# Optimization experiments

Hardware: AMD Instinct MI355X
Metric: run time of the kernel (lower is better)

The kernel has to match this reference:

```python
import jax, jax.numpy as jnp
import numpy as np

N, D, E = 16384, 1024, 8

def setup_inputs() -> dict:
    key = jax.random.key(0)
    ks = jax.random.split(key, 5)
    s = 1.0 / np.sqrt(D)
    return {
        "x": jax.random.normal(ks[0], (N, D), dtype=jnp.float32),
        "router_w": jax.random.uniform(ks[1], (E, D), jnp.float32, -s, s),   # torch Linear weight [out,in]
        "router_b": jax.random.uniform(ks[2], (E,), jnp.float32, -s, s),
        "expert_w": jax.random.uniform(ks[3], (E, D, D), jnp.float32, -s, s),  # [E, out, in]
        "expert_b": jax.random.uniform(ks[4], (E, D), jnp.float32, -s, s),
    }

def reference(x, router_w, router_b, expert_w, expert_b):
    # Router: logits -> softmax -> argmax (argmax of softmax == argmax of logits)
    logits = x @ router_w.T + router_b            # [N, E]
    top = jnp.argmax(logits, axis=-1)             # [N]
    # Compute all expert outputs (vectorized grouped GEMM), then select top-1.
    # Faithful to the torch loop: output is the raw expert output, NOT gate-scaled.
    xe = jnp.einsum('nd,eod->neo', x, expert_w) + expert_b[None, :, :]  # [N, E, D]
    out = jnp.take_along_axis(xe, top[:, None, None], axis=1)[:, 0, :]  # [N, D]
    return out
```

## Files before the change

kernel.cpp:

```cpp
#include <hip/hip_runtime.h>
#include <hip/hip_bf16.h>


#define NTOK 16384
#define DIM  1024
#define NEXP 8

#define AS1 __attribute__((address_space(1)))
#define AS3 __attribute__((address_space(3)))

typedef __bf16 bf16x8 __attribute__((ext_vector_type(8)));
typedef float  f32x4  __attribute__((ext_vector_type(4)));

__device__ __forceinline__ unsigned int f2bf(float f) {
  unsigned int u = __builtin_bit_cast(unsigned int, f);
  u += 0x7FFFu + ((u >> 16) & 1u);
  return u >> 16;
}

__global__ __launch_bounds__(256) void k_router(const float* __restrict__ x,
                                                const float* __restrict__ rw,
                                                const float* __restrict__ rb,
                                                unsigned short* __restrict__ xbf,
                                                int* __restrict__ top) {
  __shared__ float wlds[NEXP * DIM];
  const int tid = threadIdx.x;
  const int lane = tid & 63;
  const int wave = tid >> 6;
#pragma unroll
  for (int i = 0; i < 8; ++i)
    ((float4*)wlds)[tid + 256 * i] = ((const float4*)rw)[tid + 256 * i];
  __syncthreads();

  const int ea = lane & 7;
  const float bias = rb[ea];

#pragma unroll 1
  for (int tp = 0; tp < 2; ++tp) {
    const int nA = (blockIdx.x << 4) + (wave << 2) + (tp << 1);
    const int nB = nA + 1;

    float4 xa[4], xb[4];
#pragma unroll
    for (int j = 0; j < 4; ++j) {
      xa[j] = *(const float4*)(x + ((size_t)nA << 10) + (j << 8) + (lane << 2));
      xb[j] = *(const float4*)(x + ((size_t)nB << 10) + (j << 8) + (lane << 2));
    }

#pragma unroll
    for (int j = 0; j < 4; ++j) {
      uint2 sa, sb;
      sa.x = f2bf(xa[j].x) | (f2bf(xa[j].y) << 16);
      sa.y = f2bf(xa[j].z) | (f2bf(xa[j].w) << 16);
      sb.x = f2bf(xb[j].x) | (f2bf(xb[j].y) << 16);
      sb.y = f2bf(xb[j].z) | (f2bf(xb[j].w) << 16);
      *(uint2*)(xbf + ((size_t)nA << 10) + (j << 8) + (lane << 2)) = sa;
      *(uint2*)(xbf + ((size_t)nB << 10) + (j << 8) + (lane << 2)) = sb;
    }

    double pA[8] = {}, pB[8] = {};
#pragma unroll
    for (int j = 0; j < 4; ++j) {
#pragma unroll
      for (int e = 0; e < 8; ++e) {
        float4 wv = *(const float4*)&wlds[e * 1024 + (j << 8) + (lane << 2)];
        pA[e] += (double)xa[j].x * (double)wv.x;
        pA[e] += (double)xa[j].y * (double)wv.y;
        pA[e] += (double)xa[j].z * (double)wv.z;
        pA[e] += (double)xa[j].w * (double)wv.w;
        pB[e] += (double)xb[j].x * (double)wv.x;
        pB[e] += (double)xb[j].y * (double)wv.y;
        pB[e] += (double)xb[j].z * (double)wv.z;
        pB[e] += (double)xb[j].w * (double)wv.w;
      }
      __builtin_amdgcn_sched_barrier(0);
    }

    float qA[8], qB[8];
#pragma unroll
    for (int e = 0; e < 8; ++e) { qA[e] = (float)pA[e]; qB[e] = (float)pB[e]; }
#pragma unroll
    for (int e = 0; e < 8; ++e) {
      qA[e] += __shfl_xor(qA[e], 1);
      qB[e] += __shfl_xor(qB[e], 1);
      qA[e] += __shfl_xor(qA[e], 2);
      qB[e] += __shfl_xor(qB[e], 2);
      qA[e] += __shfl_xor(qA[e], 4);
      qB[e] += __shfl_xor(qB[e], 4);
    }
    float sA, sB;
    {
      float q0 = (ea & 1) ? qA[1] : qA[0], q1 = (ea & 1) ? qA[3] : qA[2];
      float q2 = (ea & 1) ? qA[5] : qA[4], q3 = (ea & 1) ? qA[7] : qA[6];
      float r0 = (ea & 2) ? q1 : q0, r1 = (ea & 2) ? q3 : q2;
      sA = (ea & 4) ? r1 : r0;
      q0 = (ea & 1) ? qB[1] : qB[0]; q1 = (ea & 1) ? qB[3] : qB[2];
      q2 = (ea & 1) ? qB[5] : qB[4]; q3 = (ea & 1) ? qB[7] : qB[6];
      r0 = (ea & 2) ? q1 : q0; r1 = (ea & 2) ? q3 : q2;
      sB = (ea & 4) ? r1 : r0;
    }
    sA += __shfl_xor(sA, 8);  sB += __shfl_xor(sB, 8);
    sA += __shfl_xor(sA, 16); sB += __shfl_xor(sB, 16);
    sA += __shfl_xor(sA, 32); sB += __shfl_xor(sB, 32);
    sA += bias; sB += bias;
    float bvA = sA, bvB = sB;
    int biA = ea, biB = ea;
#pragma unroll
    for (int mask = 1; mask <= 4; mask <<= 1) {
      float ovA = __shfl_xor(bvA, mask), ovB = __shfl_xor(bvB, mask);
      int oiA = __shfl_xor(biA, mask), oiB = __shfl_xor(biB, mask);
      if (ovA > bvA || (ovA == bvA && oiA < biA)) { bvA = ovA; biA = oiA; }
      if (ovB > bvB || (ovB == bvB && oiB < biB)) { bvB = ovB; biB = oiB; }
    }
    if (lane == 0) {
      top[nA] = biA;
      top[nB] = biB;
    }
  }
}

__global__ __launch_bounds__(1024) void k_sortconv(const float* __restrict__ ew,
                                                   unsigned short* __restrict__ wbf,
                                                   const int* __restrict__ top,
                                                   int* __restrict__ counts,
                                                   int* __restrict__ tok) {
  const int t = threadIdx.x;
  if (blockIdx.x > 0) {
    size_t i = ((size_t)(blockIdx.x - 1) * 1024 + t) * 8;
    const float4* p = (const float4*)(ew + i);
    float4 a = p[0], b = p[1];
    unsigned int w0 = f2bf(a.x) | (f2bf(a.y) << 16);
    unsigned int w1 = f2bf(a.z) | (f2bf(a.w) << 16);
    unsigned int w2 = f2bf(b.x) | (f2bf(b.y) << 16);
    unsigned int w3 = f2bf(b.z) | (f2bf(b.w) << 16);
    *(uint4*)(wbf + i) = make_uint4(w0, w1, w2, w3);
    return;
  }

  __shared__ unsigned long long wsum[2][16];
  const int lane = t & 63;
  const int wv = t >> 6;

  int4 v[4];
  const int4* tp = (const int4*)(top + t * 16);
#pragma unroll
  for (int i = 0; i < 4; ++i) v[i] = tp[i];

  unsigned long long h0 = 0, h1 = 0;
#pragma unroll
  for (int i = 0; i < 16; ++i) {
    int e = ((const int*)v)[i];
    if (e < 4) h0 += 1ull << (16 * e);
    else       h1 += 1ull << (16 * (e - 4));
  }

  unsigned long long s0 = h0, s1 = h1;
#pragma unroll
  for (int d = 1; d < 64; d <<= 1) {
    unsigned long long t0 = __shfl_up(s0, d);
    unsigned long long t1 = __shfl_up(s1, d);
    if (lane >= d) { s0 += t0; s1 += t1; }
  }
  if (lane == 63) { wsum[0][wv] = s0; wsum[1][wv] = s1; }
  __syncthreads();

  unsigned long long base0 = 0, base1 = 0;
#pragma unroll
  for (int i = 0; i < 15; ++i) {
    if (i < wv) { base0 += wsum[0][i]; base1 += wsum[1][i]; }
  }
  unsigned long long b0 = base0 + s0 - h0;
  unsigned long long b1 = base1 + s1 - h1;

  if (t == 1023) {
    unsigned long long i0 = base0 + s0, i1 = base1 + s1;
#pragma unroll
    for (int e = 0; e < 4; ++e) counts[e] = (int)((i0 >> (16 * e)) & 0xFFFF);
#pragma unroll
    for (int e = 0; e < 4; ++e) counts[4 + e] = (int)((i1 >> (16 * e)) & 0xFFFF);
  }
#pragma unroll
  for (int i = 0; i < 16; ++i) {
    int e = ((const int*)v)[i];
    int pos;
    if (e < 4) {
      pos = (int)((b0 >> (16 * e)) & 0xFFFF);
      b0 += 1ull << (16 * e);
    } else {
      int f = e - 4;
      pos = (int)((b1 >> (16 * f)) & 0xFFFF);
      b1 += 1ull << (16 * f);
    }
    tok[(e << 14) + pos] = t * 16 + i;
  }
}

__global__ __launch_bounds__(512, 2) void k_gemm(const unsigned short* __restrict__ xbf,
                                                 const unsigned short* __restrict__ wbf,
                                                 const float* __restrict__ eb,
                                                 const int* __restrict__ counts,
                                                 const int* __restrict__ tokall,
                                                 float* __restrict__ out) {
  const int bid = blockIdx.x;
  const int e = bid & 7;
  const int loc = bid >> 3;
  const int cb = loc & 7;
  const int t = loc >> 3;
  const int c = counts[e];
  if (t * 128 >= c) return;
  const int n0 = cb << 7;
  const int* tok = tokall + (e << 14);
  const int tid = threadIdx.x;
  const int lane = tid & 63;
  const int w = tid >> 6;
  const int wr = w >> 2;
  const int wn = w & 3;

  __shared__ unsigned short As[2][128 * 64];
  __shared__ unsigned short Bs[2][128 * 64];

  const int prow = tid >> 3;
  const int pchk = tid & 7;
  size_t asrc[2], bsrc[2];
  const unsigned short* wb = wbf + ((size_t)e << 20);
#pragma unroll
  for (int s = 0; s < 2; ++s) {
    int row = s * 64 + prow;
    int m = t * 128 + row;
    int g = tok[(m < c) ? m : 0];
    int l = pchk ^ (row & 7);
    asrc[s] = (size_t)g * DIM + (size_t)l * 8;
    bsrc[s] = (size_t)(n0 + row) * DIM + (size_t)l * 8;
  }

  f32x4 acc[4][2] = {};

  int aoff[2][4], boff[2][2];
#pragma unroll
  for (int h = 0; h < 2; ++h) {
#pragma unroll
    for (int m = 0; m < 4; ++m) {
      int row = wr * 64 + m * 16 + (lane & 15);
      int p = (h * 4 + (lane >> 4)) ^ (row & 7);
      aoff[h][m] = row * 64 + p * 8;
    }
#pragma unroll
    for (int n = 0; n < 2; ++n) {
      int rowb = wn * 32 + n * 16 + (lane & 15);
      int pb = (h * 4 + (lane >> 4)) ^ (rowb & 7);
      boff[h][n] = rowb * 64 + pb * 8;
    }
  }

  auto stage = [&](int b, int k0) {
#pragma unroll
    for (int s = 0; s < 2; ++s) {
      __builtin_amdgcn_global_load_lds(
          (const AS1 unsigned int*)(xbf + asrc[s] + k0),
          (AS3 unsigned int*)(&As[b][s * 4096 + w * 512]),
          16, 0, 0);
      __builtin_amdgcn_global_load_lds(
          (const AS1 unsigned int*)(wb + bsrc[s] + k0),
          (AS3 unsigned int*)(&Bs[b][s * 4096 + w * 512]),
          16, 0, 0);
    }
  };

  stage(0, 0);
  for (int k = 0; k < 16; ++k) {
    if (k < 15) {
      stage((k + 1) & 1, (k + 1) * 64);
      asm volatile("s_waitcnt vmcnt(4)" ::: "memory");
    } else {
      asm volatile("s_waitcnt vmcnt(0)" ::: "memory");
    }
    __builtin_amdgcn_s_barrier();
    __builtin_amdgcn_sched_barrier(0);
    const unsigned short* Ab = As[k & 1];
    const unsigned short* Bb = Bs[k & 1];
#pragma unroll
    for (int h = 0; h < 2; ++h) {
      bf16x8 af[4], bfr[2];
#pragma unroll
      for (int m = 0; m < 4; ++m) af[m] = *(const bf16x8*)&Ab[aoff[h][m]];
#pragma unroll
      for (int n = 0; n < 2; ++n) bfr[n] = *(const bf16x8*)&Bb[boff[h][n]];
#pragma unroll
      for (int m = 0; m < 4; ++m)
#pragma unroll
        for (int n = 0; n < 2; ++n)
          acc[m][n] = __builtin_amdgcn_mfma_f32_16x16x32_bf16(af[m], bfr[n], acc[m][n], 0, 0, 0);
    }
    __builtin_amdgcn_s_barrier();
  }

  const int colb = n0 + wn * 32 + (lane & 15);
  float bias[2];
#pragma unroll
  for (int n = 0; n < 2; ++n) bias[n] = eb[(e << 10) + colb + n * 16];
#pragma unroll
  for (int m = 0; m < 4; ++m) {
    int rbase = t * 128 + wr * 64 + m * 16 + ((lane >> 4) << 2);
#pragma unroll
    for (int r = 0; r < 4; ++r) {
      int mm = rbase + r;
      if (mm < c) {
        int g = tok[mm];
        float* op = out + ((size_t)g << 10);
#pragma unroll
        for (int n = 0; n < 2; ++n) op[colb + n * 16] = acc[m][n][r] + bias[n];
      }
    }
  }
}

extern "C" void kernel_launch(void* const* d_in, const int* in_sizes, int n_in,
                              void* d_out, int out_size, void* d_ws, size_t ws_size,
                              hipStream_t stream) {
  const float* x  = (const float*)d_in[0];
  const float* rw = (const float*)d_in[1];
  const float* rb = (const float*)d_in[2];
  const float* ew = (const float*)d_in[3];
  const float* eb = (const float*)d_in[4];
  float* out = (float*)d_out;

  char* ws = (char*)d_ws;
  unsigned short* wbf = (unsigned short*)ws;
  unsigned short* xbf = (unsigned short*)(ws + (16u << 20));
  int* tok    = (int*)(ws + (48u << 20));
  int* counts = (int*)(ws + (48u << 20) + (1u << 19));
  int* top    = (int*)(ws + (48u << 20) + (1u << 19) + 128);

  k_router<<<NTOK / 16, 256, 0, stream>>>(x, rw, rb, xbf, top);
  k_sortconv<<<1025, 1024, 0, stream>>>(ew, wbf, top, counts, tok);
  k_gemm<<<8192, 512, 0, stream>>>(xbf, wbf, eb, counts, tok, out);
}
```

Before: 92.66 us.

## Enlarge grouped GEMM tile to 256x256 with BK=32 and new swizzled LDS layout

Expands the per-block output tile from 128x128 to 256x256, so each wave now computes a 128x64 sub-tile with 32 accumulators. The K step drops to 32 and the loop runs twice as many iterations. Two rows are packed into each 64-element LDS line under a new XOR swizzle, which keeps the LDS footprint the same. This raises arithmetic intensity and reuse of A and B fragments and cuts the grid from 8192 to 2048 blocks. In exchange it costs far more accumulator registers, may lower occupancy, wastes more work on padded rows at each expert's tail, and adds barrier overhead from the shorter K steps.

Measured after the change: 124.3 us (median of 2 runs). +34.1%, slower.

```diff
diff --git a/kernel.cpp b/kernel.cpp
--- a/kernel.cpp
+++ b/kernel.cpp
@@ -204,11 +204,11 @@
   const int bid = blockIdx.x;
   const int e = bid & 7;
   const int loc = bid >> 3;
-  const int cb = loc & 7;
-  const int t = loc >> 3;
+  const int cb = loc & 3;
+  const int t = loc >> 2;
   const int c = counts[e];
-  if (t * 128 >= c) return;
-  const int n0 = cb << 7;
+  if (t * 256 >= c) return;
+  const int n0 = cb << 8;
   const int* tok = tokall + (e << 14);
   const int tid = threadIdx.x;
   const int lane = tid & 63;
@@ -216,40 +216,40 @@
   const int wr = w >> 2;
   const int wn = w & 3;
 
-  __shared__ unsigned short As[2][128 * 64];
-  __shared__ unsigned short Bs[2][128 * 64];
-
-  const int prow = tid >> 3;
-  const int pchk = tid & 7;
+  __shared__ unsigned short As[2][8192];
+  __shared__ unsigned short Bs[2][8192];
+
   size_t asrc[2], bsrc[2];
   const unsigned short* wb = wbf + ((size_t)e << 20);
 #pragma unroll
   for (int s = 0; s < 2; ++s) {
-    int row = s * 64 + prow;
-    int m = t * 128 + row;
+    int ci = s * 512 + tid;
+    int L = ci >> 3;
+    int cc = (ci & 7) ^ (L & 7);
+    int r = 2 * L + (cc >> 2);
+    int kof = (cc & 3) * 8;
+    int m = t * 256 + r;
     int g = tok[(m < c) ? m : 0];
-    int l = pchk ^ (row & 7);
-    asrc[s] = (size_t)g * DIM + (size_t)l * 8;
-    bsrc[s] = (size_t)(n0 + row) * DIM + (size_t)l * 8;
-  }
-
-  f32x4 acc[4][2] = {};
-
-  int aoff[2][4], boff[2][2];
-#pragma unroll
-  for (int h = 0; h < 2; ++h) {
-#pragma unroll
-    for (int m = 0; m < 4; ++m) {
-      int row = wr * 64 + m * 16 + (lane & 15);
-      int p = (h * 4 + (lane >> 4)) ^ (row & 7);
-      aoff[h][m] = row * 64 + p * 8;
-    }
-#pragma unroll
-    for (int n = 0; n < 2; ++n) {
-      int rowb = wn * 32 + n * 16 + (lane & 15);
-      int pb = (h * 4 + (lane >> 4)) ^ (rowb & 7);
-      boff[h][n] = rowb * 64 + pb * 8;
-    }
+    asrc[s] = (size_t)g * DIM + kof;
+    bsrc[s] = (size_t)(n0 + r) * DIM + kof;
+  }
+
+  f32x4 acc[8][4] = {};
+
+  int aoff[8], boff[4];
+#pragma unroll
+  for (int i = 0; i < 8; ++i) {
+    int r = wr * 128 + i * 16 + (lane & 15);
+    int L = r >> 1;
+    int p = (((r & 1) << 2) + (lane >> 4)) ^ (L & 7);
+    aoff[i] = L * 64 + p * 8;
+  }
+#pragma unroll
+  for (int j = 0; j < 4; ++j) {
+    int r = wn * 64 + j * 16 + (lane & 15);
+    int L = r >> 1;
+    int p = (((r & 1) << 2) + (lane >> 4)) ^ (L & 7);
+    boff[j] = L * 64 + p * 8;
   }
 
   auto stage = [&](int b, int k0) {
@@ -257,19 +257,19 @@
     for (int s = 0; s < 2; ++s) {
       __builtin_amdgcn_global_load_lds(
           (const AS1 unsigned int*)(xbf + asrc[s] + k0),
-          (AS3 unsigned int*)(&As[b][s * 4096 + w * 512]),
+          (AS3 unsigned int*)(&As[b][s * 4096 + tid * 8]),
           16, 0, 0);
       __builtin_amdgcn_global_load_lds(
           (const AS1 unsigned int*)(wb + bsrc[s] + k0),
-          (AS3 unsigned int*)(&Bs[b][s * 4096 + w * 512]),
+          (AS3 unsigned int*)(&Bs[b][s * 4096 + tid * 8]),
           16, 0, 0);
     }
   };
 
   stage(0, 0);
-  for (int k = 0; k < 16; ++k) {
-    if (k < 15) {
-      stage((k + 1) & 1, (k + 1) * 64);
+  for (int k = 0; k < 32; ++k) {
+    if (k < 31) {
+      stage((k + 1) & 1, (k + 1) * 32);
       asm volatile("s_waitcnt vmcnt(4)" ::: "memory");
     } else {
       asm volatile("s_waitcnt vmcnt(0)" ::: "memory");
@@ -278,29 +278,26 @@
     __builtin_amdgcn_sched_barrier(0);
     const unsigned short* Ab = As[k & 1];
     const unsigned short* Bb = Bs[k & 1];
-#pragma unroll
-    for (int h = 0; h < 2; ++h) {
-      bf16x8 af[4], bfr[2];
-#pragma unroll
-      for (int m = 0; m < 4; ++m) af[m] = *(const bf16x8*)&Ab[aoff[h][m]];
-#pragma unroll
-      for (int n = 0; n < 2; ++n) bfr[n] = *(const bf16x8*)&Bb[boff[h][n]];
-#pragma unroll
-      for (int m = 0; m < 4; ++m)
-#pragma unroll
-        for (int n = 0; n < 2; ++n)
-          acc[m][n] = __builtin_amdgcn_mfma_f32_16x16x32_bf16(af[m], bfr[n], acc[m][n], 0, 0, 0);
+    bf16x8 bfr[4];
+#pragma unroll
+    for (int j = 0; j < 4; ++j) bfr[j] = *(const bf16x8*)&Bb[boff[j]];
+#pragma unroll
+    for (int i = 0; i < 8; ++i) {
+      bf16x8 af = *(const bf16x8*)&Ab[aoff[i]];
+#pragma unroll
+      for (int j = 0; j < 4; ++j)
+        acc[i][j] = __builtin_amdgcn_mfma_f32_16x16x32_bf16(af, bfr[j], acc[i][j], 0, 0, 0);
     }
     __builtin_amdgcn_s_barrier();
   }
 
-  const int colb = n0 + wn * 32 + (lane & 15);
-  float bias[2];
-#pragma unroll
-  for (int n = 0; n < 2; ++n) bias[n] = eb[(e << 10) + colb + n * 16];
-#pragma unroll
-  for (int m = 0; m < 4; ++m) {
-    int rbase = t * 128 + wr * 64 + m * 16 + ((lane >> 4) << 2);
+  const int colb = n0 + wn * 64 + (lane & 15);
+  float bias[4];
+#pragma unroll
+  for (int j = 0; j < 4; ++j) bias[j] = eb[(e << 10) + colb + j * 16];
+#pragma unroll
+  for (int i = 0; i < 8; ++i) {
+    int rbase = t * 256 + wr * 128 + i * 16 + ((lane >> 4) << 2);
 #pragma unroll
     for (int r = 0; r < 4; ++r) {
       int mm = rbase + r;
@@ -308,7 +305,7 @@
         int g = tok[mm];
         float* op = out + ((size_t)g << 10);
 #pragma unroll
-        for (int n = 0; n < 2; ++n) op[colb + n * 16] = acc[m][n][r] + bias[n];
+        for (int j = 0; j < 4; ++j) op[colb + j * 16] = acc[i][j][r] + bias[j];
       }
     }
   }
@@ -333,5 +330,5 @@
 
   k_router<<<NTOK / 16, 256, 0, stream>>>(x, rw, rb, xbf, top);
   k_sortconv<<<1025, 1024, 0, stream>>>(ew, wbf, top, counts, tok);
-  k_gemm<<<8192, 512, 0, stream>>>(xbf, wbf, eb, counts, tok, out);
-}
+  k_gemm<<<2048, 512, 0, stream>>>(xbf, wbf, eb, counts, tok, out);
+}
```

## Halve GEMM K-tile to 32 with packed two-row LDS layout

Applied to the files above, without the earlier changes.

Shrinks the per-stage K tile from 64 to 32, so the grouped expert GEMM loops 32 times instead of 16. It uses a new LDS layout that packs two 32-wide rows per 64-element line with an XOR swizzle, and each thread issues one direct-to-LDS load per operand per stage. This halves shared memory per block, and the launch bound drops its min-blocks hint, presumably so more blocks fit per CU. The cost is twice as many barriers and waitcnt syncs per tile and less MFMA work between them to hide load latency.

Measured after the change: 102.2 us. 10.3% more time.

```diff
diff --git a/kernel.cpp b/kernel.cpp
--- a/kernel.cpp
+++ b/kernel.cpp
@@ -195,12 +195,12 @@
   }
 }
 
-__global__ __launch_bounds__(512, 2) void k_gemm(const unsigned short* __restrict__ xbf,
-                                                 const unsigned short* __restrict__ wbf,
-                                                 const float* __restrict__ eb,
-                                                 const int* __restrict__ counts,
-                                                 const int* __restrict__ tokall,
-                                                 float* __restrict__ out) {
+__global__ __launch_bounds__(512) void k_gemm(const unsigned short* __restrict__ xbf,
+                                              const unsigned short* __restrict__ wbf,
+                                              const float* __restrict__ eb,
+                                              const int* __restrict__ counts,
+                                              const int* __restrict__ tokall,
+                                              float* __restrict__ out) {
   const int bid = blockIdx.x;
   const int e = bid & 7;
   const int loc = bid >> 3;
@@ -216,61 +216,56 @@
   const int wr = w >> 2;
   const int wn = w & 3;
 
-  __shared__ unsigned short As[2][128 * 64];
-  __shared__ unsigned short Bs[2][128 * 64];
-
-  const int prow = tid >> 3;
-  const int pchk = tid & 7;
-  size_t asrc[2], bsrc[2];
+  __shared__ unsigned short As[2][4096];
+  __shared__ unsigned short Bs[2][4096];
+
+  size_t asrc, bsrc;
   const unsigned short* wb = wbf + ((size_t)e << 20);
-#pragma unroll
-  for (int s = 0; s < 2; ++s) {
-    int row = s * 64 + prow;
-    int m = t * 128 + row;
+  {
+    int L = tid >> 3;
+    int cc = (tid & 7) ^ (L & 7);
+    int r = 2 * L + (cc >> 2);
+    int kof = (cc & 3) * 8;
+    int m = t * 128 + r;
     int g = tok[(m < c) ? m : 0];
-    int l = pchk ^ (row & 7);
-    asrc[s] = (size_t)g * DIM + (size_t)l * 8;
-    bsrc[s] = (size_t)(n0 + row) * DIM + (size_t)l * 8;
+    asrc = (size_t)g * DIM + kof;
+    bsrc = (size_t)(n0 + r) * DIM + kof;
   }
 
   f32x4 acc[4][2] = {};
 
-  int aoff[2][4], boff[2][2];
-#pragma unroll
-  for (int h = 0; h < 2; ++h) {
-#pragma unroll
-    for (int m = 0; m < 4; ++m) {
-      int row = wr * 64 + m * 16 + (lane & 15);
-      int p = (h * 4 + (lane >> 4)) ^ (row & 7);
-      aoff[h][m] = row * 64 + p * 8;
-    }
-#pragma unroll
-    for (int n = 0; n < 2; ++n) {
-      int rowb = wn * 32 + n * 16 + (lane & 15);
-      int pb = (h * 4 + (lane >> 4)) ^ (rowb & 7);
-      boff[h][n] = rowb * 64 + pb * 8;
-    }
+  int aoff[4], boff[2];
+#pragma unroll
+  for (int m = 0; m < 4; ++m) {
+    int r = wr * 64 + m * 16 + (lane & 15);
+    int L = r >> 1;
+    int p = (((r & 1) << 2) + (lane >> 4)) ^ (L & 7);
+    aoff[m] = L * 64 + p * 8;
+  }
+#pragma unroll
+  for (int n = 0; n < 2; ++n) {
+    int r = wn * 32 + n * 16 + (lane & 15);
+    int L = r >> 1;
+    int p = (((r & 1) << 2) + (lane >> 4)) ^ (L & 7);
+    boff[n] = L * 64 + p * 8;
   }
 
   auto stage = [&](int b, int k0) {
-#pragma unroll
-    for (int s = 0; s < 2; ++s) {
-      __builtin_amdgcn_global_load_lds(
-          (const AS1 unsigned int*)(xbf + asrc[s] + k0),
-          (AS3 unsigned int*)(&As[b][s * 4096 + w * 512]),
-          16, 0, 0);
-      __builtin_amdgcn_global_load_lds(
-          (const AS1 unsigned int*)(wb + bsrc[s] + k0),
-          (AS3 unsigned int*)(&Bs[b][s * 4096 + w * 512]),
-          16, 0, 0);
-    }
+    __builtin_amdgcn_global_load_lds(
+        (const AS1 unsigned int*)(xbf + asrc + k0),
+        (AS3 unsigned int*)(&As[b][tid * 8]),
+        16, 0, 0);
+    __builtin_amdgcn_global_load_lds(
+        (const AS1 unsigned int*)(wb + bsrc + k0),
+        (AS3 unsigned int*)(&Bs[b][tid * 8]),
+        16, 0, 0);
   };
 
   stage(0, 0);
-  for (int k = 0; k < 16; ++k) {
-    if (k < 15) {
-      stage((k + 1) & 1, (k + 1) * 64);
-      asm volatile("s_waitcnt vmcnt(4)" ::: "memory");
+  for (int k = 0; k < 32; ++k) {
+    if (k < 31) {
+      stage((k + 1) & 1, (k + 1) * 32);
+      asm volatile("s_waitcnt vmcnt(2)" ::: "memory");
     } else {
       asm volatile("s_waitcnt vmcnt(0)" ::: "memory");
     }
@@ -278,19 +273,16 @@
     __builtin_amdgcn_sched_barrier(0);
     const unsigned short* Ab = As[k & 1];
     const unsigned short* Bb = Bs[k & 1];
-#pragma unroll
-    for (int h = 0; h < 2; ++h) {
-      bf16x8 af[4], bfr[2];
-#pragma unroll
-      for (int m = 0; m < 4; ++m) af[m] = *(const bf16x8*)&Ab[aoff[h][m]];
-#pragma unroll
-      for (int n = 0; n < 2; ++n) bfr[n] = *(const bf16x8*)&Bb[boff[h][n]];
-#pragma unroll
-      for (int m = 0; m < 4; ++m)
-#pragma unroll
-        for (int n = 0; n < 2; ++n)
-          acc[m][n] = __builtin_amdgcn_mfma_f32_16x16x32_bf16(af[m], bfr[n], acc[m][n], 0, 0, 0);
-    }
+    bf16x8 af[4], bfr[2];
+#pragma unroll
+    for (int m = 0; m < 4; ++m) af[m] = *(const bf16x8*)&Ab[aoff[m]];
+#pragma unroll
+    for (int n = 0; n < 2; ++n) bfr[n] = *(const bf16x8*)&Bb[boff[n]];
+#pragma unroll
+    for (int m = 0; m < 4; ++m)
+#pragma unroll
+      for (int n = 0; n < 2; ++n)
+        acc[m][n] = __builtin_amdgcn_mfma_f32_16x16x32_bf16(af[m], bfr[n], acc[m][n], 0, 0, 0);
     __builtin_amdgcn_s_barrier();
   }
 
```

## Drop double-buffered LDS staging in expert GEMM for single-buffer loop

Applied to the files above, without the earlier changes.

Replaces the double-buffered LDS prefetch pipeline in the grouped expert GEMM with a single buffer that is loaded, synchronized, and consumed each K step. The launch-bound minimum-blocks hint is also removed. This halves shared memory per block, which may allow more resident blocks, but global-to-LDS loads no longer overlap with MFMA compute, so latency is exposed on every iteration.

New measurement: 99.61 us. 7.5% more time.

```diff
diff --git a/kernel.cpp b/kernel.cpp
--- a/kernel.cpp
+++ b/kernel.cpp
@@ -195,12 +195,12 @@
   }
 }
 
-__global__ __launch_bounds__(512, 2) void k_gemm(const unsigned short* __restrict__ xbf,
-                                                 const unsigned short* __restrict__ wbf,
-                                                 const float* __restrict__ eb,
-                                                 const int* __restrict__ counts,
-                                                 const int* __restrict__ tokall,
-                                                 float* __restrict__ out) {
+__global__ __launch_bounds__(512) void k_gemm(const unsigned short* __restrict__ xbf,
+                                              const unsigned short* __restrict__ wbf,
+                                              const float* __restrict__ eb,
+                                              const int* __restrict__ counts,
+                                              const int* __restrict__ tokall,
+                                              float* __restrict__ out) {
   const int bid = blockIdx.x;
   const int e = bid & 7;
   const int loc = bid >> 3;
@@ -216,8 +216,8 @@
   const int wr = w >> 2;
   const int wn = w & 3;
 
-  __shared__ unsigned short As[2][128 * 64];
-  __shared__ unsigned short Bs[2][128 * 64];
+  __shared__ unsigned short As[128 * 64];
+  __shared__ unsigned short Bs[128 * 64];
 
   const int prow = tid >> 3;
   const int pchk = tid & 7;
@@ -252,46 +252,33 @@
     }
   }
 
-  auto stage = [&](int b, int k0) {
+  for (int k = 0; k < 16; ++k) {
 #pragma unroll
     for (int s = 0; s < 2; ++s) {
       __builtin_amdgcn_global_load_lds(
-          (const AS1 unsigned int*)(xbf + asrc[s] + k0),
-          (AS3 unsigned int*)(&As[b][s * 4096 + w * 512]),
+          (const AS1 unsigned int*)(xbf + asrc[s] + k * 64),
+          (AS3 unsigned int*)(&As[s * 4096 + w * 512]),
           16, 0, 0);
       __builtin_amdgcn_global_load_lds(
-          (const AS1 unsigned int*)(wb + bsrc[s] + k0),
-          (AS3 unsigned int*)(&Bs[b][s * 4096 + w * 512]),
+          (const AS1 unsigned int*)(wb + bsrc[s] + k * 64),
+          (AS3 unsigned int*)(&Bs[s * 4096 + w * 512]),
           16, 0, 0);
     }
-  };
-
-  stage(0, 0);
-  for (int k = 0; k < 16; ++k) {
-    if (k < 15) {
-      stage((k + 1) & 1, (k + 1) * 64);
-      asm volatile("s_waitcnt vmcnt(4)" ::: "memory");
-    } else {
-      asm volatile("s_waitcnt vmcnt(0)" ::: "memory");
-    }
-    __builtin_amdgcn_s_barrier();
-    __builtin_amdgcn_sched_barrier(0);
-    const unsigned short* Ab = As[k & 1];
-    const unsigned short* Bb = Bs[k & 1];
+    __syncthreads();
 #pragma unroll
     for (int h = 0; h < 2; ++h) {
       bf16x8 af[4], bfr[2];
 #pragma unroll
-      for (int m = 0; m < 4; ++m) af[m] = *(const bf16x8*)&Ab[aoff[h][m]];
-#pragma unroll
-      for (int n = 0; n < 2; ++n) bfr[n] = *(const bf16x8*)&Bb[boff[h][n]];
+      for (int m = 0; m < 4; ++m) af[m] = *(const bf16x8*)&As[aoff[h][m]];
+#pragma unroll
+      for (int n = 0; n < 2; ++n) bfr[n] = *(const bf16x8*)&Bs[boff[h][n]];
 #pragma unroll
       for (int m = 0; m < 4; ++m)
 #pragma unroll
         for (int n = 0; n < 2; ++n)
           acc[m][n] = __builtin_amdgcn_mfma_f32_16x16x32_bf16(af[m], bfr[n], acc[m][n], 0, 0, 0);
     }
-    __builtin_amdgcn_s_barrier();
+    if (k < 15) __syncthreads();
   }
 
   const int colb = n0 + wn * 32 + (lane & 15);
```
